# Kernel optimization log

Hardware: AMD Instinct MI355X
Metric: run time of the kernel (lower is better)

## Reference

```python
import jax, jax.numpy as jnp
import numpy as np

B, T, E, H, C = 64, 512, 512, 1024, 32
FORGET_BIAS = 1.0


def setup_inputs() -> dict:
    key = jax.random.key(0)
    ks = jax.random.split(key, 6)
    x = jax.random.normal(ks[0], (B, T, E), dtype=jnp.float32)
    # one-hot labels (softmax_cross_entropy_with_logits expects a distribution)
    y_idx = jax.random.randint(ks[1], (B,), 0, C)
    y = jax.nn.one_hot(y_idx, C, dtype=jnp.float32)
    seqlen = jnp.full((B,), T, dtype=jnp.int32)  # unused by dynamic_rnn in source
    # BasicLSTMCell kernel: concat([x, h]) @ W + b, gates split as i, j, f, o
    W = jax.random.normal(ks[2], (E + H, 4 * H), dtype=jnp.float32) * 0.02
    b = jnp.zeros((4 * H,), dtype=jnp.float32)
    out_W = jax.random.normal(ks[3], (H, C), dtype=jnp.float32)
    out_b = jax.random.normal(ks[4], (C,), dtype=jnp.float32)
    return {"x": x, "y": y, "seqlen": seqlen, "W": W, "b": b,
            "out_W": out_W, "out_b": out_b}


def lstm_last_output(x, W, b):
    # x: [B, T, E]; returns h_T: [B, H] (== outputs[:, -1] of dynamic_rnn)
    Bn = x.shape[0]
    Hn = W.shape[1] // 4

    def step(carry, xt):
        c, h = carry
        gates = jnp.concatenate([xt, h], axis=1) @ W + b  # [B, 4H]
        i, j, f, o = jnp.split(gates, 4, axis=1)
        new_c = c * jax.nn.sigmoid(f + FORGET_BIAS) + jax.nn.sigmoid(i) * jnp.tanh(j)
        new_h = jnp.tanh(new_c) * jax.nn.sigmoid(o)
        return (new_c, new_h), None

    init = (jnp.zeros((Bn, Hn), x.dtype), jnp.zeros((Bn, Hn), x.dtype))
    (_, h_last), _ = jax.lax.scan(step, init, jnp.swapaxes(x, 0, 1))  # scan over T
    return h_last


def reference(x, y, seqlen, W, b, out_W, out_b):
    h_last = lstm_last_output(x, W, b)
    pred = h_last @ out_W + out_b                    # logits [B, C]
    pred_softmax = jax.nn.softmax(pred, axis=-1)
    log_p = jax.nn.log_softmax(pred, axis=-1)
    cost = jnp.mean(-jnp.sum(y * log_p, axis=-1))    # mean softmax CE
    return pred, pred_softmax, cost
```

## Files before the change

### kernel.cpp

```cpp
#include <hip/hip_runtime.h>
#include <hip/hip_bf16.h>


#define Bb 64
#define Tt 512
#define Ee 512
#define Hh 1024
#define Cc 32
#define G4 4096
#define NKS 48
#define NBLK 128
#define HIDB 8
#define FPAD 32
#define NREP 16
#define SBMASK "0x187"

typedef __attribute__((ext_vector_type(8))) short short8;
typedef __attribute__((ext_vector_type(4))) float f32x4;

__device__ __forceinline__ unsigned short f2bf(float f) {
  __hip_bfloat16 h = __float2bfloat16(f);
  union { __hip_bfloat16 h; unsigned short u; } cv; cv.h = h; return cv.u;
}
static __device__ __forceinline__ float fsig(float x) { return 1.0f / (1.0f + __expf(-x)); }
static __device__ __forceinline__ float ftanhf(float x) {
  float e = __expf(-2.0f * fabsf(x));
  float t = (1.0f - e) / (1.0f + e);
  return copysignf(t, x);
}

__global__ __launch_bounds__(256) void transpose_x_kernel(const float* __restrict__ x,
                                                          unsigned short* __restrict__ xT) {
  const int bid = blockIdx.x;
  const int row = bid >> 9, t = bid & (Tt - 1);
  const int e = threadIdx.x * 2;
  const float* src = x + ((size_t)row * Tt + t) * Ee + e;
  float2 v = *(const float2*)src;
  ushort2 o; o.x = f2bf(v.x); o.y = f2bf(v.y);
  *(ushort2*)(xT + ((size_t)t * Bb + row) * Ee + e) = o;
}

__global__ __launch_bounds__(64) void pack_w_kernel(const float* __restrict__ W,
                                                    unsigned short* __restrict__ Wpk) {
  const int fid = blockIdx.x;
  const int l = threadIdx.x;
  const int blk = fid / 96, rem = fid % 96;
  const int tau = rem / 48, ks = rem % 48;
  const int c = l & 15;
  const int col = (2 * tau + (c >> 3)) * Hh + blk * HIDB + (c & 7);
  const int k0 = ks * 32 + (l >> 4) * 8;
  short8 v;
#pragma unroll
  for (int i = 0; i < 8; i++) v[i] = (short)f2bf(W[(size_t)(k0 + i) * G4 + col]);
  *(short8*)(Wpk + ((size_t)fid * 64 + l) * 8) = v;
}

__global__ __launch_bounds__(256) void init_state_kernel(unsigned short* __restrict__ h0,
                                                         int* __restrict__ flg) {
  int i = blockIdx.x * 256 + threadIdx.x;
  h0[i] = 0;
  if (i < 4 * NBLK * FPAD + 4 * NREP * FPAD) flg[i] = 0;
}

__global__ __launch_bounds__(256, 1) void lstm_persist(
    const unsigned short* __restrict__ xT, const unsigned short* __restrict__ Wpk,
    const float* __restrict__ bias,
    unsigned short* __restrict__ hseq,
    float* __restrict__ h_f32, int* __restrict__ flg) {
  const int bc = blockIdx.x;
  const int tid = threadIdx.x;
  const int wv = tid >> 6, ln = tid & 63;

  int* epoch = flg + 4 * NBLK * FPAD;

  if (bc == NBLK) {
    int* flgw2 = flg + wv * NBLK * FPAD;
    int* ep = epoch + wv * NREP * FPAD;
    int cur = 0;
    while (cur < Tt - 1) {
      int a = __hip_atomic_load(flgw2 + ln * FPAD,        __ATOMIC_RELAXED, __HIP_MEMORY_SCOPE_AGENT);
      int b = __hip_atomic_load(flgw2 + (ln + 64) * FPAD, __ATOMIC_RELAXED, __HIP_MEMORY_SCOPE_AGENT);
      int m = a < b ? a : b;
#pragma unroll
      for (int off = 32; off >= 1; off >>= 1) {
        int o = __shfl_xor(m, off);
        m = o < m ? o : m;
      }
      if (m > cur) {
        cur = m;
        if (ln < NREP)
          __hip_atomic_store(ep + ln * FPAD, cur, __ATOMIC_RELAXED, __HIP_MEMORY_SCOPE_AGENT);
      }
    }
    return;
  }

  __shared__ short8 Wl[2 * NKS * 64];

  {
    const short8* src = (const short8*)Wpk + (size_t)bc * (2 * NKS * 64);
    for (int i = tid; i < 2 * NKS * 64; i += 256) Wl[i] = src[i];
  }

  const int c = ln & 15, kg = ln >> 4;
  const int arow = wv * 16 + c;
  const int rbase = wv * 16 + kg * 4;
  const int hid = bc * HIDB + (c & 7);
  const bool lo = (c < 8);
  const float bi = bias[hid], bj = bias[Hh + hid];
  const float bff = bias[2 * Hh + hid], bo = bias[3 * Hh + hid];
  float cstate[4] = {0.f, 0.f, 0.f, 0.f};

  __syncthreads();

  const short8* W0 = Wl;
  const short8* W1 = Wl + NKS * 64;

  short8 wx0[16], wx1[16];
#pragma unroll
  for (int kk = 0; kk < 16; kk++) { wx0[kk] = W0[kk * 64 + ln]; wx1[kk] = W1[kk * 64 + ln]; }

  int* flgw = flg + wv * NBLK * FPAD;
  int* myslot = flgw + bc * FPAD;
  int* myep = epoch + (wv * NREP + (bc & (NREP - 1))) * FPAD;

  f32x4 xa0, xa1;
  {
    const unsigned short* xr = xT + ((size_t)0 * Bb + arow) * Ee + kg * 8;
    f32x4 a0 = {0.f,0.f,0.f,0.f}, a1 = {0.f,0.f,0.f,0.f};
#pragma unroll
    for (int kk = 0; kk < 16; kk++) {
      short8 a = *(const short8*)(xr + kk * 32);
      a0 = __builtin_amdgcn_mfma_f32_16x16x32_bf16(a, wx0[kk], a0, 0, 0, 0);
      a1 = __builtin_amdgcn_mfma_f32_16x16x32_bf16(a, wx1[kk], a1, 0, 0, 0);
    }
    xa0 = a0; xa1 = a1;
  }

  for (int t = 0; t < Tt; t++) {
    while (__hip_atomic_load(myep, __ATOMIC_RELAXED, __HIP_MEMORY_SCOPE_AGENT) < t) { }
    asm volatile("" ::: "memory");

    const unsigned short* hr = hseq + (size_t)t * (NBLK * Bb * HIDB) + kg * 512 + arow * 8;
    short8 f[32];
#pragma unroll
    for (int kk = 0; kk < 32; kk++) f[kk] = *(const short8*)(hr + kk * 2048);

    f32x4 a0 = xa0, a1 = xa1;
    asm volatile("s_waitcnt vmcnt(24)" ::: "memory");
    __builtin_amdgcn_sched_barrier(0x187);
#pragma unroll
    for (int kk = 0; kk < 8; kk++) {
      a0 = __builtin_amdgcn_mfma_f32_16x16x32_bf16(f[kk], W0[(16 + kk) * 64 + ln], a0, 0, 0, 0);
      a1 = __builtin_amdgcn_mfma_f32_16x16x32_bf16(f[kk], W1[(16 + kk) * 64 + ln], a1, 0, 0, 0);
    }
    asm volatile("s_waitcnt vmcnt(16)" ::: "memory");
    __builtin_amdgcn_sched_barrier(0x187);
#pragma unroll
    for (int kk = 8; kk < 16; kk++) {
      a0 = __builtin_amdgcn_mfma_f32_16x16x32_bf16(f[kk], W0[(16 + kk) * 64 + ln], a0, 0, 0, 0);
      a1 = __builtin_amdgcn_mfma_f32_16x16x32_bf16(f[kk], W1[(16 + kk) * 64 + ln], a1, 0, 0, 0);
    }
    asm volatile("s_waitcnt vmcnt(8)" ::: "memory");
    __builtin_amdgcn_sched_barrier(0x187);
#pragma unroll
    for (int kk = 16; kk < 24; kk++) {
      a0 = __builtin_amdgcn_mfma_f32_16x16x32_bf16(f[kk], W0[(16 + kk) * 64 + ln], a0, 0, 0, 0);
      a1 = __builtin_amdgcn_mfma_f32_16x16x32_bf16(f[kk], W1[(16 + kk) * 64 + ln], a1, 0, 0, 0);
    }
    asm volatile("s_waitcnt vmcnt(0)" ::: "memory");
    __builtin_amdgcn_sched_barrier(0x187);
#pragma unroll
    for (int kk = 24; kk < 32; kk++) {
      a0 = __builtin_amdgcn_mfma_f32_16x16x32_bf16(f[kk], W0[(16 + kk) * 64 + ln], a0, 0, 0, 0);
      a1 = __builtin_amdgcn_mfma_f32_16x16x32_bf16(f[kk], W1[(16 + kk) * 64 + ln], a1, 0, 0, 0);
    }

    if (t < Tt - 1) {
      unsigned long long* hob = (unsigned long long*)hseq
                                + (size_t)(t + 1) * (NBLK * Bb * HIDB / 4)
                                + bc * (Bb * HIDB / 4);
#pragma unroll
      for (int r = 0; r < 4; r++) {
        const float p0 = a0[r], p1 = a1[r];
        const float s0 = __shfl_xor(p0, 8), s1 = __shfl_xor(p1, 8);
        const float gi = (lo ? p0 : s0) + bi;
        const float gj = (lo ? s0 : p0) + bj;
        const float gf = (lo ? p1 : s1) + bff;
        const float go = (lo ? s1 : p1) + bo;
        const float cn = cstate[r] * fsig(gf + 1.0f) + fsig(gi) * ftanhf(gj);
        cstate[r] = cn;
        const float hn = ftanhf(cn) * fsig(go);
        unsigned short us = f2bf(hn);
        unsigned short ps = (unsigned short)__shfl_xor((int)us, 1);
        unsigned int hw = (unsigned)us | ((unsigned)ps << 16);
        unsigned int p2 = (unsigned)__shfl_xor((int)hw, 2);
        unsigned long long hq = (unsigned long long)hw | ((unsigned long long)p2 << 32);
        if (lo && !(c & 3))
          __hip_atomic_store(hob + (rbase + r) * 2 + (c >> 2),
                             hq, __ATOMIC_RELAXED, __HIP_MEMORY_SCOPE_AGENT);
      }
      asm volatile("" ::: "memory");
      const unsigned short* xr = xT + ((size_t)(t + 1) * Bb + arow) * Ee + kg * 8;
      short8 xl[16];
#pragma unroll
      for (int kk = 0; kk < 16; kk++) xl[kk] = *(const short8*)(xr + kk * 32);
      asm volatile("s_waitcnt vmcnt(16)" ::: "memory");
      __builtin_amdgcn_sched_barrier(0x187);
      if (ln == 0)
        __hip_atomic_store(myslot, t + 1, __ATOMIC_RELAXED, __HIP_MEMORY_SCOPE_AGENT);
      {
        f32x4 b0 = {0.f,0.f,0.f,0.f}, b1 = {0.f,0.f,0.f,0.f};
#pragma unroll
        for (int kk = 0; kk < 16; kk++) {
          b0 = __builtin_amdgcn_mfma_f32_16x16x32_bf16(xl[kk], wx0[kk], b0, 0, 0, 0);
          b1 = __builtin_amdgcn_mfma_f32_16x16x32_bf16(xl[kk], wx1[kk], b1, 0, 0, 0);
        }
        xa0 = b0; xa1 = b1;
      }
    } else {
      float hnew[4];
#pragma unroll
      for (int r = 0; r < 4; r++) {
        const float p0 = a0[r], p1 = a1[r];
        const float s0 = __shfl_xor(p0, 8), s1 = __shfl_xor(p1, 8);
        const float gi = (lo ? p0 : s0) + bi;
        const float gj = (lo ? s0 : p0) + bj;
        const float gf = (lo ? p1 : s1) + bff;
        const float go = (lo ? s1 : p1) + bo;
        const float cn = cstate[r] * fsig(gf + 1.0f) + fsig(gi) * ftanhf(gj);
        cstate[r] = cn;
        hnew[r] = ftanhf(cn) * fsig(go);
      }
      if (lo) {
#pragma unroll
        for (int r = 0; r < 4; r++) h_f32[(rbase + r) * Hh + hid] = hnew[r];
      }
    }
  }
}

__global__ __launch_bounds__(256) void classifier_kernel(
    const float* __restrict__ h, const float* __restrict__ outW,
    const float* __restrict__ outb, const float* __restrict__ y,
    float* __restrict__ out, float* __restrict__ losses) {
  __shared__ float red[256];
  const int brow = blockIdx.x;
  const int tid = threadIdx.x;
  const int cc = tid & 31;
  const int part = tid >> 5;
  const float* hr = h + brow * Hh;
  float p = 0.f;
  for (int k = part * 128; k < part * 128 + 128; k++)
    p += hr[k] * outW[k * Cc + cc];
  red[tid] = p;
  __syncthreads();
  if (part < 4) red[tid] += red[tid + 128];
  __syncthreads();
  if (part < 2) red[tid] += red[tid + 64];
  __syncthreads();
  if (part < 1) red[tid] += red[tid + 32];
  __syncthreads();
  if (tid < 32) {
    const float logit = red[tid] + outb[tid];
    float m = logit;
    for (int off = 16; off >= 1; off >>= 1) m = fmaxf(m, __shfl_xor(m, off));
    const float e = __expf(logit - m);
    float s = e;
    for (int off = 16; off >= 1; off >>= 1) s += __shfl_xor(s, off);
    out[brow * Cc + tid] = logit;
    out[Bb * Cc + brow * Cc + tid] = e / s;
    const float logp = (logit - m) - __logf(s);
    float contrib = y[brow * Cc + tid] * logp;
    for (int off = 16; off >= 1; off >>= 1) contrib += __shfl_xor(contrib, off);
    if (tid == 0) losses[brow] = -contrib;
  }
}

__global__ __launch_bounds__(64) void finalize_kernel(const float* __restrict__ losses,
                                                      float* __restrict__ out) {
  float v = losses[threadIdx.x];
  for (int off = 32; off >= 1; off >>= 1) v += __shfl_down(v, off);
  if (threadIdx.x == 0) out[2 * Bb * Cc] = v * (1.0f / Bb);
}

extern "C" void kernel_launch(void* const* d_in, const int* in_sizes, int n_in,
                              void* d_out, int out_size, void* d_ws, size_t ws_size,
                              hipStream_t stream) {
  const float* x    = (const float*)d_in[0];
  const float* y    = (const float*)d_in[1];
  const float* W    = (const float*)d_in[3];
  const float* bias = (const float*)d_in[4];
  const float* outW = (const float*)d_in[5];
  const float* outb = (const float*)d_in[6];
  float* out = (float*)d_out;

  char* wsp = (char*)d_ws;
  size_t off = 0;
  auto walloc = [&](size_t bytes) -> void* {
    void* p = wsp + off;
    off += (bytes + 255) & ~(size_t)255;
    return p;
  };
  unsigned short* xT   = (unsigned short*)walloc((size_t)Bb * Tt * Ee * 2);
  unsigned short* Wpk  = (unsigned short*)walloc((size_t)NBLK * 2 * NKS * 64 * 16);
  unsigned short* hseq = (unsigned short*)walloc((size_t)Tt * Bb * Hh * 2);
  float* hf     = (float*)walloc((size_t)Bb * Hh * 4);
  float* losses = (float*)walloc(256);
  int* flg      = (int*)walloc((4 * NBLK * FPAD + 4 * NREP * FPAD) * 4);
  (void)ws_size; (void)in_sizes; (void)n_in; (void)out_size;

  transpose_x_kernel<<<Bb * Tt, 256, 0, stream>>>(x, xT);
  pack_w_kernel<<<NBLK * 2 * NKS, 64, 0, stream>>>(W, Wpk);
  init_state_kernel<<<(Bb * Hh) / 256, 256, 0, stream>>>(hseq, flg);

  lstm_persist<<<NBLK + 1, 256, 0, stream>>>(xT, Wpk, bias, hseq, hf, flg);

  classifier_kernel<<<Bb, 256, 0, stream>>>(hf, outW, outb, y, out, losses);
  finalize_kernel<<<1, 64, 0, stream>>>(losses, out);
}
```

Measured before the change: 3.019 ms.

## Replace aggregator-block epoch barrier with direct per-wave polling of all flags

Removes the dedicated aggregator block that reduced all 128 per-block flags and broadcast an epoch counter to replicated slots. Each wave now polls all 128 producer flags directly (two per lane) and sleeps briefly between polls. This drops one hop of cross-block latency from every timestep's barrier. In exchange it puts far more polling traffic on the shared flag lines, and s_sleep may add wake-up latency.

```diff
diff --git a/kernel.cpp b/kernel.cpp
--- a/kernel.cpp
+++ b/kernel.cpp
@@ -12,8 +12,6 @@
 #define NBLK 128
 #define HIDB 8
 #define FPAD 32
-#define NREP 16
-#define SBMASK "0x187"
 
 typedef __attribute__((ext_vector_type(8))) short short8;
 typedef __attribute__((ext_vector_type(4))) float f32x4;
@@ -59,7 +57,7 @@
                                                          int* __restrict__ flg) {
   int i = blockIdx.x * 256 + threadIdx.x;
   h0[i] = 0;
-  if (i < 4 * NBLK * FPAD + 4 * NREP * FPAD) flg[i] = 0;
+  if (i < 4 * NBLK * FPAD) flg[i] = 0;
 }
 
 __global__ __launch_bounds__(256, 1) void lstm_persist(
@@ -71,30 +69,6 @@
   const int tid = threadIdx.x;
   const int wv = tid >> 6, ln = tid & 63;
 
-  int* epoch = flg + 4 * NBLK * FPAD;
-
-  if (bc == NBLK) {
-    int* flgw2 = flg + wv * NBLK * FPAD;
-    int* ep = epoch + wv * NREP * FPAD;
-    int cur = 0;
-    while (cur < Tt - 1) {
-      int a = __hip_atomic_load(flgw2 + ln * FPAD,        __ATOMIC_RELAXED, __HIP_MEMORY_SCOPE_AGENT);
-      int b = __hip_atomic_load(flgw2 + (ln + 64) * FPAD, __ATOMIC_RELAXED, __HIP_MEMORY_SCOPE_AGENT);
-      int m = a < b ? a : b;
-#pragma unroll
-      for (int off = 32; off >= 1; off >>= 1) {
-        int o = __shfl_xor(m, off);
-        m = o < m ? o : m;
-      }
-      if (m > cur) {
-        cur = m;
-        if (ln < NREP)
-          __hip_atomic_store(ep + ln * FPAD, cur, __ATOMIC_RELAXED, __HIP_MEMORY_SCOPE_AGENT);
-      }
-    }
-    return;
-  }
-
   __shared__ short8 Wl[2 * NKS * 64];
 
   {
@@ -122,7 +96,8 @@
 
   int* flgw = flg + wv * NBLK * FPAD;
   int* myslot = flgw + bc * FPAD;
-  int* myep = epoch + (wv * NREP + (bc & (NREP - 1))) * FPAD;
+  int* slot0 = flgw + ln * FPAD;
+  int* slot1 = flgw + (ln + 64) * FPAD;
 
   f32x4 xa0, xa1;
   {
@@ -138,7 +113,12 @@
   }
 
   for (int t = 0; t < Tt; t++) {
-    while (__hip_atomic_load(myep, __ATOMIC_RELAXED, __HIP_MEMORY_SCOPE_AGENT) < t) { }
+    for (;;) {
+      int v0 = __hip_atomic_load(slot0, __ATOMIC_RELAXED, __HIP_MEMORY_SCOPE_AGENT);
+      int v1 = __hip_atomic_load(slot1, __ATOMIC_RELAXED, __HIP_MEMORY_SCOPE_AGENT);
+      if (v0 >= t && v1 >= t) break;
+      __builtin_amdgcn_s_sleep(1);
+    }
     asm volatile("" ::: "memory");
 
     const unsigned short* hr = hseq + (size_t)t * (NBLK * Bb * HIDB) + kg * 512 + arow * 8;
@@ -307,14 +287,14 @@
   unsigned short* hseq = (unsigned short*)walloc((size_t)Tt * Bb * Hh * 2);
   float* hf     = (float*)walloc((size_t)Bb * Hh * 4);
   float* losses = (float*)walloc(256);
-  int* flg      = (int*)walloc((4 * NBLK * FPAD + 4 * NREP * FPAD) * 4);
+  int* flg      = (int*)walloc(4 * NBLK * FPAD * 4);
   (void)ws_size; (void)in_sizes; (void)n_in; (void)out_size;
 
   transpose_x_kernel<<<Bb * Tt, 256, 0, stream>>>(x, xT);
   pack_w_kernel<<<NBLK * 2 * NKS, 64, 0, stream>>>(W, Wpk);
   init_state_kernel<<<(Bb * Hh) / 256, 256, 0, stream>>>(hseq, flg);
 
-  lstm_persist<<<NBLK + 1, 256, 0, stream>>>(xT, Wpk, bias, hseq, hf, flg);
+  lstm_persist<<<NBLK, 256, 0, stream>>>(xT, Wpk, bias, hseq, hf, flg);
 
   classifier_kernel<<<Bb, 256, 0, stream>>>(hf, outW, outb, y, out, losses);
   finalize_kernel<<<1, 64, 0, stream>>>(losses, out);
```

New measurement: 3.229 ms. +7.0%, slower.

## Duplicate aggregator blocks for epoch broadcast and split MFMA accumulator chains

Applied to the files above, without the earlier changes.

Launches two aggregator blocks instead of one. Each aggregator watches the per-block progress flags and publishes the epoch to its own set of 8 replica slots, and worker blocks poll both copies and proceed when either is ready, so a slow aggregator is less likely to stall a step. The recurrent MFMA chain is also split into two independent accumulators that are summed at the end, which shortens the serial dependency. This costs an extra block, more polling traffic, and a slightly different floating-point summation order.

```diff
diff --git a/kernel.cpp b/kernel.cpp
--- a/kernel.cpp
+++ b/kernel.cpp
@@ -13,7 +13,6 @@
 #define HIDB 8
 #define FPAD 32
 #define NREP 16
-#define SBMASK "0x187"
 
 typedef __attribute__((ext_vector_type(8))) short short8;
 typedef __attribute__((ext_vector_type(4))) float f32x4;
@@ -73,9 +72,10 @@
 
   int* epoch = flg + 4 * NBLK * FPAD;
 
-  if (bc == NBLK) {
+  if (bc >= NBLK) {
+    const int ag = bc - NBLK;
     int* flgw2 = flg + wv * NBLK * FPAD;
-    int* ep = epoch + wv * NREP * FPAD;
+    int* ep = epoch + (wv * NREP + ag * 8) * FPAD;
     int cur = 0;
     while (cur < Tt - 1) {
       int a = __hip_atomic_load(flgw2 + ln * FPAD,        __ATOMIC_RELAXED, __HIP_MEMORY_SCOPE_AGENT);
@@ -88,7 +88,7 @@
       }
       if (m > cur) {
         cur = m;
-        if (ln < NREP)
+        if (ln < 8)
           __hip_atomic_store(ep + ln * FPAD, cur, __ATOMIC_RELAXED, __HIP_MEMORY_SCOPE_AGENT);
       }
     }
@@ -122,7 +122,8 @@
 
   int* flgw = flg + wv * NBLK * FPAD;
   int* myslot = flgw + bc * FPAD;
-  int* myep = epoch + (wv * NREP + (bc & (NREP - 1))) * FPAD;
+  int* myep0 = epoch + (wv * NREP + (bc & 7)) * FPAD;
+  int* myep1 = epoch + (wv * NREP + 8 + (bc & 7)) * FPAD;
 
   f32x4 xa0, xa1;
   {
@@ -138,7 +139,11 @@
   }
 
   for (int t = 0; t < Tt; t++) {
-    while (__hip_atomic_load(myep, __ATOMIC_RELAXED, __HIP_MEMORY_SCOPE_AGENT) < t) { }
+    for (;;) {
+      int e0 = __hip_atomic_load(myep0, __ATOMIC_RELAXED, __HIP_MEMORY_SCOPE_AGENT);
+      int e1 = __hip_atomic_load(myep1, __ATOMIC_RELAXED, __HIP_MEMORY_SCOPE_AGENT);
+      if (e0 >= t || e1 >= t) break;
+    }
     asm volatile("" ::: "memory");
 
     const unsigned short* hr = hseq + (size_t)t * (NBLK * Bb * HIDB) + kg * 512 + arow * 8;
@@ -147,6 +152,7 @@
     for (int kk = 0; kk < 32; kk++) f[kk] = *(const short8*)(hr + kk * 2048);
 
     f32x4 a0 = xa0, a1 = xa1;
+    f32x4 b0 = {0.f,0.f,0.f,0.f}, b1 = {0.f,0.f,0.f,0.f};
     asm volatile("s_waitcnt vmcnt(24)" ::: "memory");
     __builtin_amdgcn_sched_barrier(0x187);
 #pragma unroll
@@ -165,16 +171,17 @@
     __builtin_amdgcn_sched_barrier(0x187);
 #pragma unroll
     for (int kk = 16; kk < 24; kk++) {
-      a0 = __builtin_amdgcn_mfma_f32_16x16x32_bf16(f[kk], W0[(16 + kk) * 64 + ln], a0, 0, 0, 0);
-      a1 = __builtin_amdgcn_mfma_f32_16x16x32_bf16(f[kk], W1[(16 + kk) * 64 + ln], a1, 0, 0, 0);
+      b0 = __builtin_amdgcn_mfma_f32_16x16x32_bf16(f[kk], W0[(16 + kk) * 64 + ln], b0, 0, 0, 0);
+      b1 = __builtin_amdgcn_mfma_f32_16x16x32_bf16(f[kk], W1[(16 + kk) * 64 + ln], b1, 0, 0, 0);
     }
     asm volatile("s_waitcnt vmcnt(0)" ::: "memory");
     __builtin_amdgcn_sched_barrier(0x187);
 #pragma unroll
     for (int kk = 24; kk < 32; kk++) {
-      a0 = __builtin_amdgcn_mfma_f32_16x16x32_bf16(f[kk], W0[(16 + kk) * 64 + ln], a0, 0, 0, 0);
-      a1 = __builtin_amdgcn_mfma_f32_16x16x32_bf16(f[kk], W1[(16 + kk) * 64 + ln], a1, 0, 0, 0);
-    }
+      b0 = __builtin_amdgcn_mfma_f32_16x16x32_bf16(f[kk], W0[(16 + kk) * 64 + ln], b0, 0, 0, 0);
+      b1 = __builtin_amdgcn_mfma_f32_16x16x32_bf16(f[kk], W1[(16 + kk) * 64 + ln], b1, 0, 0, 0);
+    }
+    a0 += b0; a1 += b1;
 
     if (t < Tt - 1) {
       unsigned long long* hob = (unsigned long long*)hseq
@@ -210,13 +217,13 @@
       if (ln == 0)
         __hip_atomic_store(myslot, t + 1, __ATOMIC_RELAXED, __HIP_MEMORY_SCOPE_AGENT);
       {
-        f32x4 b0 = {0.f,0.f,0.f,0.f}, b1 = {0.f,0.f,0.f,0.f};
+        f32x4 c0 = {0.f,0.f,0.f,0.f}, c1 = {0.f,0.f,0.f,0.f};
 #pragma unroll
         for (int kk = 0; kk < 16; kk++) {
-          b0 = __builtin_amdgcn_mfma_f32_16x16x32_bf16(xl[kk], wx0[kk], b0, 0, 0, 0);
-          b1 = __builtin_amdgcn_mfma_f32_16x16x32_bf16(xl[kk], wx1[kk], b1, 0, 0, 0);
+          c0 = __builtin_amdgcn_mfma_f32_16x16x32_bf16(xl[kk], wx0[kk], c0, 0, 0, 0);
+          c1 = __builtin_amdgcn_mfma_f32_16x16x32_bf16(xl[kk], wx1[kk], c1, 0, 0, 0);
         }
-        xa0 = b0; xa1 = b1;
+        xa0 = c0; xa1 = c1;
       }
     } else {
       float hnew[4];
@@ -314,7 +321,7 @@
   pack_w_kernel<<<NBLK * 2 * NKS, 64, 0, stream>>>(W, Wpk);
   init_state_kernel<<<(Bb * Hh) / 256, 256, 0, stream>>>(hseq, flg);
 
-  lstm_persist<<<NBLK + 1, 256, 0, stream>>>(xT, Wpk, bias, hseq, hf, flg);
+  lstm_persist<<<NBLK + 2, 256, 0, stream>>>(xT, Wpk, bias, hseq, hf, flg);
 
   classifier_kernel<<<Bb, 256, 0, stream>>>(hf, outW, outb, y, out, losses);
   finalize_kernel<<<1, 64, 0, stream>>>(losses, out);
```

Result: faster. 2.721 ms (median of 2 runs) (-9.9%).
